# Kernel tuning notes

Measured on AMD Instinct MI355X. Metric: run time of the kernel, lower is better.

## Reference

```python
import jax, jax.numpy as jnp
import numpy as np

B, S, D, H = 4, 2048, 1024, 16
DK = D // H


def setup_inputs() -> dict:
    key = jax.random.key(0)
    ks = jax.random.split(key, 12)
    s = 1.0 / np.sqrt(D)
    return {
        "query": jax.random.normal(ks[0], (B, S, D), jnp.float32),
        "key": jax.random.normal(ks[1], (B, S, D), jnp.float32),
        "value": jax.random.normal(ks[2], (B, S, D), jnp.float32),
        "mask": jax.random.randint(ks[3], (B, S), 0, 2, jnp.int32),
        "wq": jax.random.normal(ks[4], (D, D), jnp.float32) * s,
        "bq": jnp.zeros((D,), jnp.float32),
        "wk": jax.random.normal(ks[5], (D, D), jnp.float32) * s,
        "bk": jnp.zeros((D,), jnp.float32),
        "wv": jax.random.normal(ks[6], (D, D), jnp.float32) * s,
        "bv": jnp.zeros((D,), jnp.float32),
        "wo": jax.random.normal(ks[7], (D, D), jnp.float32) * s,
        "bo": jnp.zeros((D,), jnp.float32),
    }


def reference(query, key, value, mask, wq, bq, wk, bk, wv, bv, wo, bo):
    # torch Linear: y = x @ W.T + b
    def proj(x, w, b):
        y = jnp.einsum('bsd,ed->bse', x, w) + b
        return y.reshape(B, S, H, DK).transpose(0, 2, 1, 3)  # [B,H,S,DK]

    q = proj(query, wq, bq)
    k = proj(key, wk, bk)
    v = proj(value, wv, bv)

    scores = jnp.einsum('bhqd,bhkd->bhqk', q, k) / jnp.sqrt(jnp.float32(DK))
    m = mask[:, None, None, :]  # [B,1,1,S_kv]
    scores = jnp.where(m == 0, jnp.float32(-1e9), scores)
    attn = jax.nn.softmax(scores, axis=-1)  # dropout p=0.0 (eval)
    out = jnp.einsum('bhqk,bhkd->bhqd', attn, v)
    out = out.transpose(0, 2, 1, 3).reshape(B, S, D)
    return jnp.einsum('bsd,ed->bse', out, wo) + bo
```

## Files before the change

### kernel.cpp

```cpp
#include <hip/hip_runtime.h>
#include <hip/hip_bf16.h>

typedef __bf16 bf16;
typedef bf16 bf16x2 __attribute__((ext_vector_type(2)));
typedef bf16 bf16x4 __attribute__((ext_vector_type(4)));
typedef bf16 bf16x8 __attribute__((ext_vector_type(8)));
typedef float f32x4 __attribute__((ext_vector_type(4)));
typedef float f32x16 __attribute__((ext_vector_type(16)));
typedef unsigned int u32;
typedef u32 u32x4 __attribute__((ext_vector_type(4)));

#define MFMA16(A,B,C) __builtin_amdgcn_mfma_f32_16x16x32_bf16(A,B,C,0,0,0)
#define MFMA32(A,B,C) __builtin_amdgcn_mfma_f32_32x32x16_bf16(A,B,C,0,0,0)

__device__ __forceinline__ void gld_lds16(const void* g, void* l) {
  __builtin_amdgcn_global_load_lds(
      (const __attribute__((address_space(1))) void*)g,
      (__attribute__((address_space(3))) void*)l, 16, 0, 0);
}

__global__ void cast3_kernel(const float* __restrict__ s0, const float* __restrict__ s1,
                             const float* __restrict__ s2,
                             bf16* __restrict__ d0, bf16* __restrict__ d1, bf16* __restrict__ d2) {
  const int which = blockIdx.x >> 13;
  const int i = (blockIdx.x & 8191) * 256 + threadIdx.x;
  const float* s = which == 0 ? s0 : which == 1 ? s1 : s2;
  bf16* d = which == 0 ? d0 : which == 1 ? d1 : d2;
  float4 v = ((const float4*)s)[i];
  bf16x4 o;
  o[0] = (bf16)v.x; o[1] = (bf16)v.y; o[2] = (bf16)v.z; o[3] = (bf16)v.w;
  *(bf16x4*)(d + (size_t)i * 4) = o;
}

__global__ void cast4_kernel(const float* __restrict__ s0, const float* __restrict__ s1,
                             const float* __restrict__ s2, const float* __restrict__ s3,
                             bf16* __restrict__ d0, bf16* __restrict__ d1,
                             bf16* __restrict__ d2, bf16* __restrict__ d3) {
  const int which = blockIdx.x >> 10;
  const int i = (blockIdx.x & 1023) * 256 + threadIdx.x;
  const float* s = which == 0 ? s0 : which == 1 ? s1 : which == 2 ? s2 : s3;
  bf16* d = which == 0 ? d0 : which == 1 ? d1 : which == 2 ? d2 : d3;
  float4 v = ((const float4*)s)[i];
  bf16x4 o;
  o[0] = (bf16)v.x; o[1] = (bf16)v.y; o[2] = (bf16)v.z; o[3] = (bf16)v.w;
  *(bf16x4*)(d + (size_t)i * 4) = o;
}

template<int OUT_MODE>
__global__ __launch_bounds__(256) void gemm_bt_kernel(
    const bf16* __restrict__ A, const bf16* __restrict__ Bm,
    const float* __restrict__ bias, void* __restrict__ Cout,
    int M, int N, int K, float scale)
{
  __shared__ bf16 sA[2][128 * 32];
  __shared__ bf16 sB[2][128 * 32];
  const int t = threadIdx.x;
  const int lane = t & 63, w = t >> 6;
  const int wr = w >> 1, wc = w & 1;
  const int g = lane >> 4, c = lane & 15;
  const int bm = blockIdx.y, bn = blockIdx.x;

  f32x4 acc[4][4] = {};

  const int NT = K >> 5;
  const int arow = t >> 2;
  const int acol = (t & 3) * 8;
  const bf16* aBase = A + (size_t)(bm * 128) * K;
  const bf16* bBase = Bm + (size_t)(bn * 128) * K;

  auto stage = [&](int buf, int kt) {
    const int k0 = kt * 32;
#pragma unroll
    for (int i = 0; i < 2; ++i) {
      const int row = arow + i * 64;
      gld_lds16(aBase + (size_t)row * K + k0 + acol, &sA[buf][(i * 256 + t) * 8]);
      gld_lds16(bBase + (size_t)row * K + k0 + acol, &sB[buf][(i * 256 + t) * 8]);
    }
  };

  stage(0, 0);
  __syncthreads();
  int cur = 0;
  for (int kt = 0; kt < NT; ++kt) {
    if (kt + 1 < NT) stage(cur ^ 1, kt + 1);
    bf16x8 af[4], bfr[4];
#pragma unroll
    for (int m = 0; m < 4; ++m)
      af[m] = *(const bf16x8*)&sA[cur][(wr * 64 + m * 16 + c) * 32 + g * 8];
#pragma unroll
    for (int n = 0; n < 4; ++n)
      bfr[n] = *(const bf16x8*)&sB[cur][(wc * 64 + n * 16 + c) * 32 + g * 8];
    __builtin_amdgcn_s_setprio(1);
#pragma unroll
    for (int m = 0; m < 4; ++m)
#pragma unroll
      for (int n = 0; n < 4; ++n)
        acc[m][n] = MFMA16(af[m], bfr[n], acc[m][n]);
    __builtin_amdgcn_s_setprio(0);
    __syncthreads();
    cur ^= 1;
  }

#pragma unroll
  for (int n = 0; n < 4; ++n) {
    const int col = bn * 128 + wc * 64 + n * 16 + c;
    const float bv = bias[col];
#pragma unroll
    for (int m = 0; m < 4; ++m) {
#pragma unroll
      for (int r = 0; r < 4; ++r) {
        const int row = bm * 128 + wr * 64 + m * 16 + g * 4 + r;
        const float val = (acc[m][n][r] + bv) * scale;
        if (OUT_MODE == 0) {
          ((bf16*)Cout)[(size_t)row * N + col] = (bf16)val;
        } else if (OUT_MODE == 1) {
          const int bb = row >> 11, s = row & 2047;
          ((bf16*)Cout)[((size_t)(bb * 1024 + col)) * 2048 + s] = (bf16)val;
        } else {
          ((float*)Cout)[(size_t)row * N + col] = val;
        }
      }
    }
  }
}

__global__ __launch_bounds__(256) void attn_kernel(
    const bf16* __restrict__ Qp, const bf16* __restrict__ Kp, const bf16* __restrict__ Vt,
    const int* __restrict__ mask, bf16* __restrict__ Out)
{
  __shared__ bf16 sK[2][64 * 64];
  __shared__ bf16 sV[2][64 * 64];

  const int bh = blockIdx.x;
  const int b = bh >> 4, h = bh & 15;
  const int t = threadIdx.x, lane = t & 63, w = t >> 6;
  const int q32 = lane & 31, hi = lane >> 5;
  const int q0 = blockIdx.y * 128 + w * 32;

  const char* kBase = (const char*)(Kp + (size_t)(b * 2048) * 1024 + h * 64);
  const char* vBase = (const char*)(Vt + (size_t)(bh * 64) * 2048);

  auto stageKV = [&](int buf, int kt) {
#pragma unroll
    for (int i = 0; i < 2; ++i) {
      const int idx = i * 256 + t;
      const int row = idx >> 3;
      const int cb = ((t & 7) * 16) ^ ((row & 7) << 4);
      gld_lds16(kBase + (size_t)(kt * 64 + row) * 2048 + cb, (char*)sK[buf] + idx * 16);
      gld_lds16(vBase + (size_t)row * 4096 + kt * 128 + cb, (char*)sV[buf] + idx * 16);
    }
  };

  bf16x8 qf[4];
  const bf16* qrow = Qp + (size_t)(b * 2048 + q0 + q32) * 1024 + h * 64;
#pragma unroll
  for (int ks = 0; ks < 4; ++ks)
    qf[ks] = *(const bf16x8*)&qrow[ks * 16 + hi * 8];

  float mrun = -1e30f, lrun = 0.f;
  f32x16 aco[2] = {};

  const int* mrow = mask + b * 2048;

  stageKV(0, 0);
  __syncthreads();
  int cur = 0;
  for (int kt = 0; kt < 32; ++kt) {
    if (kt + 1 < 32) stageKV(cur ^ 1, kt + 1);

    f32x16 st[2];
#pragma unroll
    for (int kf = 0; kf < 2; ++kf)
#pragma unroll
      for (int q4 = 0; q4 < 4; ++q4) {
        const int4 mm = *(const int4*)&mrow[kt * 64 + kf * 32 + q4 * 8 + hi * 4];
        st[kf][q4 * 4 + 0] = mm.x ? 0.0f : -1e9f;
        st[kf][q4 * 4 + 1] = mm.y ? 0.0f : -1e9f;
        st[kf][q4 * 4 + 2] = mm.z ? 0.0f : -1e9f;
        st[kf][q4 * 4 + 3] = mm.w ? 0.0f : -1e9f;
      }

#pragma unroll
    for (int ks = 0; ks < 4; ++ks) {
      bf16x8 k0f, k1f;
      {
        const int row = q32;
        const int byt = (row * 128 + ks * 32 + hi * 16) ^ ((row & 7) << 4);
        k0f = *(const bf16x8*)((const char*)sK[cur] + byt);
      }
      {
        const int row = 32 + q32;
        const int byt = (row * 128 + ks * 32 + hi * 16) ^ ((row & 7) << 4);
        k1f = *(const bf16x8*)((const char*)sK[cur] + byt);
      }
      __builtin_amdgcn_s_setprio(1);
      st[0] = MFMA32(k0f, qf[ks], st[0]);
      st[1] = MFMA32(k1f, qf[ks], st[1]);
      __builtin_amdgcn_s_setprio(0);
    }

    float t0 = fmaxf(st[0][0], st[0][1]), t1 = fmaxf(st[0][2], st[0][3]);
    float t2 = fmaxf(st[1][0], st[1][1]), t3 = fmaxf(st[1][2], st[1][3]);
#pragma unroll
    for (int i = 4; i < 16; i += 4) {
      t0 = fmaxf(t0, fmaxf(st[0][i], st[0][i + 1]));
      t1 = fmaxf(t1, fmaxf(st[0][i + 2], st[0][i + 3]));
      t2 = fmaxf(t2, fmaxf(st[1][i], st[1][i + 1]));
      t3 = fmaxf(t3, fmaxf(st[1][i + 2], st[1][i + 3]));
    }
    float tmax = fmaxf(fmaxf(t0, t1), fmaxf(t2, t3));
    tmax = fmaxf(tmax, __shfl_xor(tmax, 32, 64));
    if (!__all(tmax <= mrun + 11.5f)) {
      const float mnew = fmaxf(mrun, tmax);
      const float sc = exp2f(mrun - mnew);
      mrun = mnew;
      lrun *= sc;
      aco[0] *= sc;
      aco[1] *= sc;
    }
    float rs0 = 0.f, rs1 = 0.f, rs2 = 0.f, rs3 = 0.f;
#pragma unroll
    for (int i = 0; i < 16; i += 4) {
      float p00 = exp2f(st[0][i] - mrun),     p01 = exp2f(st[0][i + 1] - mrun);
      float p02 = exp2f(st[0][i + 2] - mrun), p03 = exp2f(st[0][i + 3] - mrun);
      float p10 = exp2f(st[1][i] - mrun),     p11 = exp2f(st[1][i + 1] - mrun);
      float p12 = exp2f(st[1][i + 2] - mrun), p13 = exp2f(st[1][i + 3] - mrun);
      st[0][i] = p00; st[0][i + 1] = p01; st[0][i + 2] = p02; st[0][i + 3] = p03;
      st[1][i] = p10; st[1][i + 1] = p11; st[1][i + 2] = p12; st[1][i + 3] = p13;
      rs0 += p00 + p01; rs1 += p02 + p03;
      rs2 += p10 + p11; rs3 += p12 + p13;
    }
    float rs = (rs0 + rs1) + (rs2 + rs3);
    rs += __shfl_xor(rs, 32, 64);
    lrun += rs;

    bf16x8 pa[4];
#pragma unroll
    for (int kf = 0; kf < 2; ++kf) {
      u32 u[4][2];
#pragma unroll
      for (int g2 = 0; g2 < 4; ++g2) {
        asm("v_cvt_pk_bf16_f32 %0, %1, %2"
            : "=v"(u[g2][0]) : "v"(st[kf][4 * g2 + 0]), "v"(st[kf][4 * g2 + 1]));
        asm("v_cvt_pk_bf16_f32 %0, %1, %2"
            : "=v"(u[g2][1]) : "v"(st[kf][4 * g2 + 2]), "v"(st[kf][4 * g2 + 3]));
      }
      u32 d0 = u[0][0], d2 = u[1][0];
      asm("v_permlane32_swap_b32 %0, %1" : "+v"(d0), "+v"(d2));
      u32 d1 = u[0][1], d3 = u[1][1];
      asm("v_permlane32_swap_b32 %0, %1" : "+v"(d1), "+v"(d3));
      u32x4 ud = {d0, d1, d2, d3};
      pa[2 * kf] = __builtin_bit_cast(bf16x8, ud);
      u32 e0 = u[2][0], e2 = u[3][0];
      asm("v_permlane32_swap_b32 %0, %1" : "+v"(e0), "+v"(e2));
      u32 e1 = u[2][1], e3 = u[3][1];
      asm("v_permlane32_swap_b32 %0, %1" : "+v"(e1), "+v"(e3));
      u32x4 ue = {e0, e1, e2, e3};
      pa[2 * kf + 1] = __builtin_bit_cast(bf16x8, ue);
    }

#pragma unroll
    for (int kk = 0; kk < 4; ++kk) {
      bf16x8 vb0, vb1;
      {
        const int row = q32;
        const int byt = (row * 128 + kk * 32 + hi * 16) ^ ((row & 7) << 4);
        vb0 = *(const bf16x8*)((const char*)sV[cur] + byt);
      }
      {
        const int row = 32 + q32;
        const int byt = (row * 128 + kk * 32 + hi * 16) ^ ((row & 7) << 4);
        vb1 = *(const bf16x8*)((const char*)sV[cur] + byt);
      }
      __builtin_amdgcn_s_setprio(1);
      aco[0] = MFMA32(vb0, pa[kk], aco[0]);
      aco[1] = MFMA32(vb1, pa[kk], aco[1]);
      __builtin_amdgcn_s_setprio(0);
    }

    __syncthreads();
    cur ^= 1;
  }

  const float inv = 1.0f / lrun;
  bf16* orow = Out + (size_t)(b * 2048 + q0 + q32) * 1024 + h * 64;
#pragma unroll
  for (int dkf = 0; dkf < 2; ++dkf)
#pragma unroll
    for (int q4 = 0; q4 < 4; ++q4) {
      bf16x4 o;
#pragma unroll
      for (int r4 = 0; r4 < 4; ++r4)
        o[r4] = (bf16)(aco[dkf][q4 * 4 + r4] * inv);
      *(bf16x4*)&orow[dkf * 32 + q4 * 8 + hi * 4] = o;
    }
}

extern "C" void kernel_launch(void* const* d_in, const int* in_sizes, int n_in,
                              void* d_out, int out_size, void* d_ws, size_t ws_size,
                              hipStream_t stream) {
  const float* q  = (const float*)d_in[0];
  const float* k  = (const float*)d_in[1];
  const float* v  = (const float*)d_in[2];
  const int*  msk = (const int*)d_in[3];
  const float* wq = (const float*)d_in[4];
  const float* bq = (const float*)d_in[5];
  const float* wk = (const float*)d_in[6];
  const float* bk = (const float*)d_in[7];
  const float* wv = (const float*)d_in[8];
  const float* bv = (const float*)d_in[9];
  const float* wo = (const float*)d_in[10];
  const float* bo = (const float*)d_in[11];

  bf16* ws = (bf16*)d_ws;
  const size_t NEL = 8192ull * 1024ull;
  bf16* qx  = ws;
  bf16* kx  = ws + NEL;
  bf16* vx  = ws + 2 * NEL;
  bf16* wqb = ws + 3 * NEL;
  bf16* wkb = wqb + 1048576;
  bf16* wvb = wkb + 1048576;
  bf16* wob = wvb + 1048576;
  bf16* qp  = wob + 1048576;
  bf16* kp  = qp + NEL;
  bf16* vt  = kp + NEL;
  bf16* ao  = vx;

  cast3_kernel<<<24576, 256, 0, stream>>>(q, k, v, qx, kx, vx);
  cast4_kernel<<<4096, 256, 0, stream>>>(wq, wk, wv, wo, wqb, wkb, wvb, wob);

  const float qscale = 0.125f * 1.44269504088896f;
  dim3 gg(8, 64);
  gemm_bt_kernel<0><<<gg, 256, 0, stream>>>(qx, wqb, bq, qp, 8192, 1024, 1024, qscale);
  gemm_bt_kernel<0><<<gg, 256, 0, stream>>>(kx, wkb, bk, kp, 8192, 1024, 1024, 1.0f);
  gemm_bt_kernel<1><<<gg, 256, 0, stream>>>(vx, wvb, bv, vt, 8192, 1024, 1024, 1.0f);
  attn_kernel<<<dim3(64, 16), 256, 0, stream>>>(qp, kp, vt, msk, ao);
  gemm_bt_kernel<2><<<gg, 256, 0, stream>>>(ao, wob, bo, d_out, 8192, 1024, 1024, 1.0f);
}
```

Baseline: 448.0 us.

## Replace 128x128 GEMMs with 256x256 triple-buffered swizzled GEMM and fuse QKV launches

The 128x128 double-buffered projection GEMM is replaced by a 256x256-tile, 512-thread kernel with a three-stage LDS pipeline, explicit vmcnt waits and an XOR-swizzled LDS layout meant to avoid bank conflicts. The Q, K and V projections are merged into a single launch using blockIdx.z, and the output projection uses the same core. The goal is more reuse per loaded byte, more load/compute overlap and fewer launches. In exchange, the grid becomes small (384 and 128 blocks), which may underfill the 256 CUs, and sizes are now hardcoded to 1024.

```diff
diff --git a/kernel.cpp b/kernel.cpp
--- a/kernel.cpp
+++ b/kernel.cpp
@@ -46,79 +46,145 @@
   *(bf16x4*)(d + (size_t)i * 4) = o;
 }
 
-template<int OUT_MODE>
-__global__ __launch_bounds__(256) void gemm_bt_kernel(
-    const bf16* __restrict__ A, const bf16* __restrict__ Bm,
-    const float* __restrict__ bias, void* __restrict__ Cout,
-    int M, int N, int K, float scale)
+__device__ __forceinline__ void gemm256_core(
+    const bf16* __restrict__ aBase, const bf16* __restrict__ bBase,
+    bf16* sA, bf16* sB, f32x4 (&acc)[8][4])
 {
-  __shared__ bf16 sA[2][128 * 32];
-  __shared__ bf16 sB[2][128 * 32];
   const int t = threadIdx.x;
   const int lane = t & 63, w = t >> 6;
-  const int wr = w >> 1, wc = w & 1;
-  const int g = lane >> 4, c = lane & 15;
+  const int wr = w >> 2, wc = w & 3;
+  const int c = lane & 15, g = lane >> 4;
+
+  const int tl   = (t * 16) ^ (((t >> 3) & 7) << 4);
+  const int srow = tl >> 6;
+  const int scol = (tl & 63) >> 1;
+  const int dstE = t * 8;
+
+  auto stage = [&](int buf, int kt) {
+#pragma unroll
+    for (int r = 0; r < 2; ++r)
+      gld_lds16(aBase + (size_t)(r * 128 + srow) * 1024 + kt * 32 + scol,
+                &sA[buf * 8192 + r * 4096 + dstE]);
+#pragma unroll
+    for (int r = 0; r < 2; ++r)
+      gld_lds16(bBase + (size_t)(r * 128 + srow) * 1024 + kt * 32 + scol,
+                &sB[buf * 8192 + r * 4096 + dstE]);
+  };
+
+  auto rd = [&](const bf16* s, int row) -> bf16x8 {
+    const int phys = (row * 64 + g * 16) ^ (((row >> 1) & 7) << 4);
+    return *(const bf16x8*)((const char*)s + phys);
+  };
+
+  stage(0, 0);
+  stage(1, 1);
+
+#pragma unroll 1
+  for (int kt = 0; kt < 32; ++kt) {
+    __builtin_amdgcn_s_barrier();
+    if (kt < 30) {
+      stage((kt + 2) % 3, kt + 2);
+      asm volatile("s_waitcnt vmcnt(8)" ::: "memory");
+    } else if (kt == 30) {
+      asm volatile("s_waitcnt vmcnt(4)" ::: "memory");
+    } else {
+      asm volatile("s_waitcnt vmcnt(0)" ::: "memory");
+    }
+    __builtin_amdgcn_s_barrier();
+
+    const bf16* tA = sA + (kt % 3) * 8192;
+    const bf16* tB = sB + (kt % 3) * 8192;
+
+    bf16x8 bfr[4];
+#pragma unroll
+    for (int ni = 0; ni < 4; ++ni) bfr[ni] = rd(tB, wc * 64 + ni * 16 + c);
+    bf16x8 af[4];
+#pragma unroll
+    for (int mi = 0; mi < 4; ++mi) af[mi] = rd(tA, wr * 128 + mi * 16 + c);
+    __builtin_amdgcn_s_setprio(1);
+#pragma unroll
+    for (int mi = 0; mi < 4; ++mi)
+#pragma unroll
+      for (int ni = 0; ni < 4; ++ni)
+        acc[mi][ni] = MFMA16(af[mi], bfr[ni], acc[mi][ni]);
+    __builtin_amdgcn_s_setprio(0);
+#pragma unroll
+    for (int mi = 0; mi < 4; ++mi) af[mi] = rd(tA, wr * 128 + (mi + 4) * 16 + c);
+    __builtin_amdgcn_s_setprio(1);
+#pragma unroll
+    for (int mi = 0; mi < 4; ++mi)
+#pragma unroll
+      for (int ni = 0; ni < 4; ++ni)
+        acc[mi + 4][ni] = MFMA16(af[mi], bfr[ni], acc[mi + 4][ni]);
+    __builtin_amdgcn_s_setprio(0);
+  }
+}
+
+__global__ __launch_bounds__(512, 2) void qkv_gemm256(
+    const bf16* __restrict__ qx, const bf16* __restrict__ kx, const bf16* __restrict__ vx,
+    const bf16* __restrict__ wqb, const bf16* __restrict__ wkb, const bf16* __restrict__ wvb,
+    const float* __restrict__ bq, const float* __restrict__ bk, const float* __restrict__ bv,
+    bf16* __restrict__ qp, bf16* __restrict__ kp, bf16* __restrict__ vt, float qscale)
+{
+  __shared__ bf16 sA[3 * 8192];
+  __shared__ bf16 sB[3 * 8192];
+  const int z = blockIdx.z;
+  const bf16* A   = z == 0 ? qx  : z == 1 ? kx  : vx;
+  const bf16* Bm  = z == 0 ? wqb : z == 1 ? wkb : wvb;
+  const float* bias = z == 0 ? bq : z == 1 ? bk : bv;
   const int bm = blockIdx.y, bn = blockIdx.x;
 
-  f32x4 acc[4][4] = {};
-
-  const int NT = K >> 5;
-  const int arow = t >> 2;
-  const int acol = (t & 3) * 8;
-  const bf16* aBase = A + (size_t)(bm * 128) * K;
-  const bf16* bBase = Bm + (size_t)(bn * 128) * K;
-
-  auto stage = [&](int buf, int kt) {
-    const int k0 = kt * 32;
-#pragma unroll
-    for (int i = 0; i < 2; ++i) {
-      const int row = arow + i * 64;
-      gld_lds16(aBase + (size_t)row * K + k0 + acol, &sA[buf][(i * 256 + t) * 8]);
-      gld_lds16(bBase + (size_t)row * K + k0 + acol, &sB[buf][(i * 256 + t) * 8]);
-    }
-  };
-
-  stage(0, 0);
-  __syncthreads();
-  int cur = 0;
-  for (int kt = 0; kt < NT; ++kt) {
-    if (kt + 1 < NT) stage(cur ^ 1, kt + 1);
-    bf16x8 af[4], bfr[4];
-#pragma unroll
-    for (int m = 0; m < 4; ++m)
-      af[m] = *(const bf16x8*)&sA[cur][(wr * 64 + m * 16 + c) * 32 + g * 8];
-#pragma unroll
-    for (int n = 0; n < 4; ++n)
-      bfr[n] = *(const bf16x8*)&sB[cur][(wc * 64 + n * 16 + c) * 32 + g * 8];
-    __builtin_amdgcn_s_setprio(1);
-#pragma unroll
-    for (int m = 0; m < 4; ++m)
-#pragma unroll
-      for (int n = 0; n < 4; ++n)
-        acc[m][n] = MFMA16(af[m], bfr[n], acc[m][n]);
-    __builtin_amdgcn_s_setprio(0);
-    __syncthreads();
-    cur ^= 1;
+  f32x4 acc[8][4] = {};
+  gemm256_core(A + (size_t)(bm * 256) * 1024, Bm + (size_t)(bn * 256) * 1024, sA, sB, acc);
+
+  const int t = threadIdx.x, lane = t & 63, w = t >> 6;
+  const int wr = w >> 2, wc = w & 3, c = lane & 15, g = lane >> 4;
+  const float sc = z == 0 ? qscale : 1.0f;
+  bf16* Cb = z == 0 ? qp : kp;
+#pragma unroll
+  for (int ni = 0; ni < 4; ++ni) {
+    const int col = bn * 256 + wc * 64 + ni * 16 + c;
+    const float bvv = bias[col];
+#pragma unroll
+    for (int mi = 0; mi < 8; ++mi) {
+#pragma unroll
+      for (int r4 = 0; r4 < 4; ++r4) {
+        const int row = bm * 256 + wr * 128 + mi * 16 + g * 4 + r4;
+        const float val = (acc[mi][ni][r4] + bvv) * sc;
+        if (z == 2) {
+          const int bb = row >> 11, s = row & 2047;
+          vt[((size_t)(bb * 1024 + col)) * 2048 + s] = (bf16)val;
+        } else {
+          Cb[(size_t)row * 1024 + col] = (bf16)val;
+        }
+      }
+    }
   }
-
-#pragma unroll
-  for (int n = 0; n < 4; ++n) {
-    const int col = bn * 128 + wc * 64 + n * 16 + c;
-    const float bv = bias[col];
-#pragma unroll
-    for (int m = 0; m < 4; ++m) {
-#pragma unroll
-      for (int r = 0; r < 4; ++r) {
-        const int row = bm * 128 + wr * 64 + m * 16 + g * 4 + r;
-        const float val = (acc[m][n][r] + bv) * scale;
-        if (OUT_MODE == 0) {
-          ((bf16*)Cout)[(size_t)row * N + col] = (bf16)val;
-        } else if (OUT_MODE == 1) {
-          const int bb = row >> 11, s = row & 2047;
-          ((bf16*)Cout)[((size_t)(bb * 1024 + col)) * 2048 + s] = (bf16)val;
-        } else {
-          ((float*)Cout)[(size_t)row * N + col] = val;
-        }
+}
+
+__global__ __launch_bounds__(512, 2) void out_gemm256(
+    const bf16* __restrict__ A, const bf16* __restrict__ Bm,
+    const float* __restrict__ bias, float* __restrict__ Cout)
+{
+  __shared__ bf16 sA[3 * 8192];
+  __shared__ bf16 sB[3 * 8192];
+  const int bm = blockIdx.y, bn = blockIdx.x;
+
+  f32x4 acc[8][4] = {};
+  gemm256_core(A + (size_t)(bm * 256) * 1024, Bm + (size_t)(bn * 256) * 1024, sA, sB, acc);
+
+  const int t = threadIdx.x, lane = t & 63, w = t >> 6;
+  const int wr = w >> 2, wc = w & 3, c = lane & 15, g = lane >> 4;
+#pragma unroll
+  for (int ni = 0; ni < 4; ++ni) {
+    const int col = bn * 256 + wc * 64 + ni * 16 + c;
+    const float bvv = bias[col];
+#pragma unroll
+    for (int mi = 0; mi < 8; ++mi) {
+#pragma unroll
+      for (int r4 = 0; r4 < 4; ++r4) {
+        const int row = bm * 256 + wr * 128 + mi * 16 + g * 4 + r4;
+        Cout[(size_t)row * 1024 + col] = acc[mi][ni][r4] + bvv;
       }
     }
   }
@@ -330,10 +396,8 @@
   cast4_kernel<<<4096, 256, 0, stream>>>(wq, wk, wv, wo, wqb, wkb, wvb, wob);
 
   const float qscale = 0.125f * 1.44269504088896f;
-  dim3 gg(8, 64);
-  gemm_bt_kernel<0><<<gg, 256, 0, stream>>>(qx, wqb, bq, qp, 8192, 1024, 1024, qscale);
-  gemm_bt_kernel<0><<<gg, 256, 0, stream>>>(kx, wkb, bk, kp, 8192, 1024, 1024, 1.0f);
-  gemm_bt_kernel<1><<<gg, 256, 0, stream>>>(vx, wvb, bv, vt, 8192, 1024, 1024, 1.0f);
+  qkv_gemm256<<<dim3(4, 32, 3), 512, 0, stream>>>(qx, kx, vx, wqb, wkb, wvb,
+                                                  bq, bk, bv, qp, kp, vt, qscale);
   attn_kernel<<<dim3(64, 16), 256, 0, stream>>>(qp, kp, vt, msk, ao);
-  gemm_bt_kernel<2><<<gg, 256, 0, stream>>>(ao, wob, bo, d_out, 8192, 1024, 1024, 1.0f);
-}
+  out_gemm256<<<dim3(4, 32), 512, 0, stream>>>(ao, wob, bo, (float*)d_out);
+}
```

Result: slower. 495.1 us (+10.5%).
